# Performance work log

Measured on AMD Instinct MI355X. Metric: run time of the kernel, lower is better.

Reference implementation:

```python
import jax, jax.numpy as jnp
import numpy as np

N_SRC, N_TGT, E, L, C_OUT = 100000, 200000, 500000, 256, 2


def setup_inputs() -> dict:
    key = jax.random.key(0)
    ks = jax.random.split(key, 10)
    s = 1.0 / np.sqrt(L)
    return {
        "pos_source": jax.random.normal(ks[0], (N_SRC, 3), jnp.float32),
        "pos_target": jax.random.normal(ks[1], (N_TGT, 3), jnp.float32),
        "latents": jax.random.normal(ks[2], (N_SRC, L), jnp.float32),
        "row": jax.random.randint(ks[3], (E,), 0, N_TGT),
        "col": jax.random.randint(ks[4], (E,), 0, N_SRC),
        "W_in": jax.random.normal(ks[5], (L + 3, L), jnp.float32) * s,
        "b_in": jnp.zeros((L,), jnp.float32),
        "W1": jax.random.normal(ks[6], (L, L), jnp.float32) * s,
        "b1": jnp.zeros((L,), jnp.float32),
        "W2": jax.random.normal(ks[7], (L, L), jnp.float32) * s,
        "b2": jnp.zeros((L,), jnp.float32),
        "W_out": jax.random.normal(ks[8], (L, C_OUT), jnp.float32) * s,
        "b_out": jnp.zeros((C_OUT,), jnp.float32),
    }


def reference(pos_source, pos_target, latents, row, col,
              W_in, b_in, W1, b1, W2, b2, W_out, b_out):
    # gather relative positions and latents per neighbor pair: [E, 3], [E, L]
    pos_rel = pos_target[row] - pos_source[col]
    x = jnp.concatenate([latents[col], pos_rel], axis=1)  # [E, L+3]
    x = x @ W_in + b_in                                   # fc_in
    x = jax.nn.relu(x) @ W1 + b1                          # mlp layer 0 (act first)
    x = jax.nn.relu(x) @ W2 + b2                          # mlp layer 1
    x = x @ W_out + b_out                                 # fc_out (no activation)
    return x[:, 0]                                        # predictions
```

## Files before the change

### kernel.cpp

```cpp
#include <hip/hip_runtime.h>
#include <hip/hip_bf16.h>
#include <stdint.h>

typedef __attribute__((ext_vector_type(8))) short bf16x8;
typedef __attribute__((ext_vector_type(4))) float f32x4;

#define NSRC 100000
#define WIN_OFF 0
#define W1P_OFF (128*1024)
#define BU_OFF  (256*1024)
#define SS_OFF  (BU_OFF + 2048)
#define Y_OFF   (264*1024)

#define PAIRB 1040
#define XBYTES (32*PAIRB)
#define POFF(r) (((r)>>1)*PAIRB + ((r)&1)*512)

#define AS3U32(p) ((__attribute__((address_space(3))) uint32_t*)(uintptr_t)(p))
#define AS1U32(p) ((const __attribute__((address_space(1))) uint32_t*)(uintptr_t)(p))

__global__ __launch_bounds__(256) void pack_kernel(
    const float* __restrict__ Win, const float* __restrict__ W1,
    const float* __restrict__ W2, const float* __restrict__ Wout,
    const float* __restrict__ b1, const float* __restrict__ b2,
    const float* __restrict__ b_out, char* __restrict__ wp)
{
    const int t = threadIdx.x, blk = blockIdx.x;
    if (blk < 16) {
        const float* W = (blk < 8) ? Win : W1;
        char* dst = wp + ((blk < 8) ? WIN_OFF : W1P_OFF);
        const int c = blk & 7;
        #pragma unroll
        for (int q = 0; q < 4; ++q) {
            union { bf16x8 v; __hip_bfloat16 h[8]; } u;
            #pragma unroll
            for (int j = 0; j < 8; ++j)
                u.h[j] = __float2bfloat16(W[(size_t)(c*32 + q*8 + j)*256 + t]);
            *(bf16x8*)(dst + c*16384 + t*64 + q*16) = u.v;
        }
    } else if (blk < 24) {
        __shared__ float w0s[256];
        w0s[t] = Wout[t*2];
        __syncthreads();
        const int b = blk - 16, fl = t >> 3, sub = t & 7, f = b*32 + fl;
        const float* row = W2 + (size_t)f*256 + sub*32;
        float p = 0.f;
        #pragma unroll
        for (int j = 0; j < 32; ++j) p += row[j]*w0s[sub*32 + j];
        p += __shfl_xor(p,1); p += __shfl_xor(p,2); p += __shfl_xor(p,4);
        if (sub == 0) {
            float2 v; v.x = b1[f]; v.y = p;
            *(float2*)(wp + BU_OFF + f*8) = v;
        }
    } else {
        __shared__ float rb[4];
        float v = b2[t]*Wout[t*2];
        v += __shfl_xor(v,1); v += __shfl_xor(v,2); v += __shfl_xor(v,4);
        v += __shfl_xor(v,8); v += __shfl_xor(v,16); v += __shfl_xor(v,32);
        if ((t&63) == 0) rb[t>>6] = v;
        __syncthreads();
        if (t == 0) *(float*)(wp + SS_OFF) = rb[0]+rb[1]+rb[2]+rb[3] + b_out[0];
    }
}

__global__ __launch_bounds__(256, 2) void precompute_y(
    const float* __restrict__ latents, const float* __restrict__ b_in,
    const char* __restrict__ wp, char* __restrict__ Yc)
{
    __shared__ __align__(16) char Xs[XBYTES];
    __shared__ float binS[256];
    const int tid = threadIdx.x, wave = tid >> 6, lane = tid & 63;
    const int q = lane >> 4, lm = lane & 15;

    bf16x8 wA[4][8];
    {
        const char* wb = wp + WIN_OFF;
        #pragma unroll
        for (int mt = 0; mt < 4; ++mt) {
            const int m = wave*64 + mt*16 + lm;
            #pragma unroll
            for (int c = 0; c < 8; ++c)
                wA[mt][c] = *(const bf16x8*)(wb + c*16384 + m*64 + q*16);
        }
    }
    binS[tid] = b_in[tid];

    const int ntY = (NSRC + 63) / 64;
    for (int tile = blockIdx.x; tile < ntY; tile += 512) {
        const int base = tile*64;
        {
            const int r = tid & 63, h = tid >> 6;
            int srow = base + r; if (srow >= NSRC) srow = NSRC - 1;
            const float4* lp = (const float4*)(latents + (size_t)srow*256 + h*64);
            #pragma unroll
            for (int w = 0; w < 8; ++w) {
                float4 v0 = lp[w*2], v1 = lp[w*2+1];
                union { bf16x8 v; __hip_bfloat16 hh[8]; } u;
                u.hh[0]=__float2bfloat16(v0.x); u.hh[1]=__float2bfloat16(v0.y);
                u.hh[2]=__float2bfloat16(v0.z); u.hh[3]=__float2bfloat16(v0.w);
                u.hh[4]=__float2bfloat16(v1.x); u.hh[5]=__float2bfloat16(v1.y);
                u.hh[6]=__float2bfloat16(v1.z); u.hh[7]=__float2bfloat16(v1.w);
                *(bf16x8*)(Xs + POFF(r) + h*128 + w*16) = u.v;
            }
        }
        __syncthreads();
        f32x4 acc[4][4];
        #pragma unroll
        for (int mt = 0; mt < 4; ++mt)
            #pragma unroll
            for (int nt = 0; nt < 4; ++nt) acc[mt][nt] = (f32x4){0.f,0.f,0.f,0.f};
        #pragma unroll
        for (int c = 0; c < 8; ++c) {
            bf16x8 b[4];
            #pragma unroll
            for (int nt = 0; nt < 4; ++nt)
                b[nt] = *(const bf16x8*)(Xs + POFF(nt*16+lm) + c*64 + q*16);
            #pragma unroll
            for (int mt = 0; mt < 4; ++mt)
                #pragma unroll
                for (int nt = 0; nt < 4; ++nt)
                    acc[mt][nt] = __builtin_amdgcn_mfma_f32_16x16x32_bf16(wA[mt][c], b[nt], acc[mt][nt], 0,0,0);
        }
        #pragma unroll
        for (int mt = 0; mt < 4; ++mt) {
            const int f0 = wave*64 + mt*16 + q*4;
            float4 bb = *(const float4*)&binS[f0];
            float bbv[4] = {bb.x, bb.y, bb.z, bb.w};
            #pragma unroll
            for (int nt = 0; nt < 4; ++nt) {
                const int srow = base + nt*16 + lm;
                if (srow < NSRC) {
                    union { uint2 uu; __hip_bfloat16 hh[4]; } pk;
                    #pragma unroll
                    for (int rg = 0; rg < 4; ++rg)
                        pk.hh[rg] = __float2bfloat16(acc[mt][nt][rg] + bbv[rg]);
                    *(uint2*)(Yc + (size_t)srow*512 + f0*2) = pk.uu;
                }
            }
        }
        __syncthreads();
    }
}

__global__ __launch_bounds__(256, 2) void interp_main(
    const float* __restrict__ pos_src, const float* __restrict__ pos_tgt,
    const int* __restrict__ rowi, const int* __restrict__ coli,
    const float* __restrict__ Win, const char* __restrict__ wp,
    const char* __restrict__ Yc, float* __restrict__ out,
    int E, int ntiles)
{
    __shared__ __align__(16) char Xs[2][XBYTES];
    __shared__ float wposI[32][24];
    __shared__ float buS[512];
    __shared__ float posrel[2][64][4];
    __shared__ int   colsS[2][64];
    __shared__ float red[4][64];

    const int tid = threadIdx.x, wave = tid >> 6, lane = tid & 63;
    const int q = lane >> 4, lm = lane & 15;
    const int bid = blockIdx.x;

    bf16x8 wA[4][8];
    {
        const char* wb = wp + W1P_OFF;
        #pragma unroll
        for (int mt = 0; mt < 4; ++mt) {
            const int m = wave*64 + mt*16 + lm;
            #pragma unroll
            for (int c = 0; c < 8; ++c)
                wA[mt][c] = *(const bf16x8*)(wb + c*16384 + m*64 + q*16);
        }
    }
    {
        #pragma unroll
        for (int s = 0; s < 3; ++s)
            wposI[tid >> 3][s*8 + (tid & 7)] = Win[(size_t)(256+s)*256 + tid];
        *(float2*)&buS[tid*2] = *(const float2*)(wp + BU_OFF + tid*8);
    }
    const float Sv = *(const float*)(wp + SS_OFF);
    const int niter = (ntiles - bid + 511) / 512;

    #pragma unroll
    for (int ii = 0; ii < 2; ++ii) {
        if (tid < 64) {
            long tt = (long)bid + (long)ii*512; if (tt >= ntiles) tt = ntiles - 1;
            long e = tt*64 + tid; if (e >= E) e = E - 1;
            int ri = rowi[e], ci = coli[e];
            colsS[ii][tid] = ci;
            float4 pr;
            pr.x = pos_tgt[ri*3+0] - pos_src[ci*3+0];
            pr.y = pos_tgt[ri*3+1] - pos_src[ci*3+1];
            pr.z = pos_tgt[ri*3+2] - pos_src[ci*3+2];
            pr.w = 0.f;
            *(float4*)&posrel[ii][tid][0] = pr;
        }
    }
    __syncthreads();
    {
        #pragma unroll
        for (int k2 = 0; k2 < 8; ++k2) {
            const int r0 = wave*16 + k2*2;
            const int row = r0 + (lane >> 5);
            const int cv = colsS[0][row];
            const char* src = Yc + (size_t)cv*512 + (lane & 31)*16;
            __builtin_amdgcn_global_load_lds(AS1U32(src), AS3U32(Xs[0] + (r0>>1)*PAIRB), 16, 0, 0);
        }
    }

    for (int i = 0; i < niter; ++i) {
        const int p = i & 1;
        __syncthreads();

        if (i > 0 && tid < 64) {
            long e = ((long)bid + (long)(i-1)*512)*64 + tid;
            if (e < E) out[e] = red[0][tid]+red[1][tid]+red[2][tid]+red[3][tid] + Sv;
        }
        int m_ci = 0; float4 m_pr = {0.f,0.f,0.f,0.f};
        if (tid < 64) {
            long tt = (long)bid + (long)(i+2)*512; if (tt >= ntiles) tt = ntiles - 1;
            long e = tt*64 + tid; if (e >= E) e = E - 1;
            int ri = rowi[e]; m_ci = coli[e];
            m_pr.x = pos_tgt[ri*3+0] - pos_src[m_ci*3+0];
            m_pr.y = pos_tgt[ri*3+1] - pos_src[m_ci*3+1];
            m_pr.z = pos_tgt[ri*3+2] - pos_src[m_ci*3+2];
        }
        {
            const int fs = tid & 31, rb = tid >> 5;
            float w0v[8], w1v[8], w2v[8];
            {
                const float* wi = &wposI[fs][0];
                #pragma unroll
                for (int j = 0; j < 8; ++j) { w0v[j]=wi[j]; w1v[j]=wi[8+j]; w2v[j]=wi[16+j]; }
            }
            char* xb = Xs[p];
            #pragma unroll
            for (int ii2 = 0; ii2 < 8; ++ii2) {
                const int r = rb*8 + ii2;
                float4 pr = *(const float4*)&posrel[p][r][0];
                char* addr = xb + POFF(r) + fs*16;
                union { bf16x8 v; __hip_bfloat16 h[8]; } u;
                u.v = *(bf16x8*)addr;
                #pragma unroll
                for (int j = 0; j < 8; ++j) {
                    float vv = __bfloat162float(u.h[j]) + pr.x*w0v[j] + pr.y*w1v[j] + pr.z*w2v[j];
                    u.h[j] = __float2bfloat16(vv < 0.f ? 0.f : vv);
                }
                *(bf16x8*)addr = u.v;
            }
        }
        __syncthreads();

        {
            const int s = 1 - p;
            char* xb = Xs[s];
            #pragma unroll
            for (int k2 = 0; k2 < 8; ++k2) {
                const int r0 = wave*16 + k2*2;
                const int row = r0 + (lane >> 5);
                const int cv = colsS[s][row];
                const char* src = Yc + (size_t)cv*512 + (lane & 31)*16;
                __builtin_amdgcn_global_load_lds(AS1U32(src), AS3U32(xb + (r0>>1)*PAIRB), 16, 0, 0);
            }
        }
        f32x4 acc[4][4];
        #pragma unroll
        for (int mt = 0; mt < 4; ++mt)
            #pragma unroll
            for (int nt = 0; nt < 4; ++nt) acc[mt][nt] = (f32x4){0.f,0.f,0.f,0.f};
        {
            const char* xb = Xs[p];
            #pragma unroll
            for (int c = 0; c < 8; ++c) {
                bf16x8 b[4];
                #pragma unroll
                for (int nt = 0; nt < 4; ++nt)
                    b[nt] = *(const bf16x8*)(xb + POFF(nt*16+lm) + c*64 + q*16);
                #pragma unroll
                for (int mt = 0; mt < 4; ++mt)
                    #pragma unroll
                    for (int nt = 0; nt < 4; ++nt)
                        acc[mt][nt] = __builtin_amdgcn_mfma_f32_16x16x32_bf16(wA[mt][c], b[nt], acc[mt][nt], 0,0,0);
            }
        }
        float partial[4] = {0.f,0.f,0.f,0.f};
        #pragma unroll
        for (int mt = 0; mt < 4; ++mt) {
            const int f0 = wave*64 + mt*16 + q*4;
            float4 bu0 = *(const float4*)&buS[f0*2];
            float4 bu1 = *(const float4*)&buS[f0*2 + 4];
            float b1v[4] = {bu0.x, bu0.z, bu1.x, bu1.z};
            float uv[4]  = {bu0.y, bu0.w, bu1.y, bu1.w};
            #pragma unroll
            for (int nt = 0; nt < 4; ++nt)
                #pragma unroll
                for (int rg = 0; rg < 4; ++rg) {
                    float h = acc[mt][nt][rg] + b1v[rg];
                    if (h > 0.f) partial[nt] += h * uv[rg];
                }
        }
        #pragma unroll
        for (int nt = 0; nt < 4; ++nt) {
            float v = partial[nt];
            v += __shfl_xor(v, 16);
            v += __shfl_xor(v, 32);
            if (lane < 16) red[wave][nt*16 + lane] = v;
        }
        if (tid < 64) {
            colsS[p][tid] = m_ci;
            *(float4*)&posrel[p][tid][0] = m_pr;
        }
    }
    __syncthreads();
    if (tid < 64) {
        long e = ((long)bid + (long)(niter-1)*512)*64 + tid;
        if (e < E) out[e] = red[0][tid]+red[1][tid]+red[2][tid]+red[3][tid] + Sv;
    }
}

extern "C" void kernel_launch(void* const* d_in, const int* in_sizes, int n_in,
                              void* d_out, int out_size, void* d_ws, size_t ws_size,
                              hipStream_t stream)
{
    const float* pos_src = (const float*)d_in[0];
    const float* pos_tgt = (const float*)d_in[1];
    const float* latents = (const float*)d_in[2];
    const int*   rowi    = (const int*)d_in[3];
    const int*   coli    = (const int*)d_in[4];
    const float* Win     = (const float*)d_in[5];
    const float* b_in    = (const float*)d_in[6];
    const float* W1      = (const float*)d_in[7];
    const float* b1      = (const float*)d_in[8];
    const float* W2      = (const float*)d_in[9];
    const float* b2      = (const float*)d_in[10];
    const float* Wout    = (const float*)d_in[11];
    const float* b_out   = (const float*)d_in[12];
    float* out = (float*)d_out;
    const int E = in_sizes[3];
    const int ntiles = (E + 63) / 64;

    char* wp = (char*)d_ws;
    char* Yc = wp + Y_OFF;

    pack_kernel<<<25, 256, 0, stream>>>(Win, W1, W2, Wout, b1, b2, b_out, wp);
    precompute_y<<<512, 256, 0, stream>>>(latents, b_in, wp, Yc);
    interp_main<<<512, 256, 0, stream>>>(pos_src, pos_tgt, rowi, coli,
                                         Win, wp, Yc, out, E, ntiles);
}
```

Before: 311.2 us.

## Swizzle LDS tile layout and vectorize bf16 packing in interp kernels

```diff
diff --git a/kernel.cpp b/kernel.cpp
--- a/kernel.cpp
+++ b/kernel.cpp
@@ -12,12 +12,17 @@
 #define SS_OFF  (BU_OFF + 2048)
 #define Y_OFF   (264*1024)
 
-#define PAIRB 1040
-#define XBYTES (32*PAIRB)
-#define POFF(r) (((r)>>1)*PAIRB + ((r)&1)*512)
-
 #define AS3U32(p) ((__attribute__((address_space(3))) uint32_t*)(uintptr_t)(p))
 #define AS1U32(p) ((const __attribute__((address_space(1))) uint32_t*)(uintptr_t)(p))
+
+__device__ __forceinline__ int xpos(int r, int g) {
+    return (((g) & 24) | (((g) + (r)) & 7)) << 4;
+}
+
+__device__ __forceinline__ unsigned int pkbf16(float a, float b) {
+    __hip_bfloat162 h = __float22bfloat162_rn(make_float2(a, b));
+    union { __hip_bfloat162 h; unsigned int u; } c; c.h = h; return c.u;
+}
 
 __global__ __launch_bounds__(256) void pack_kernel(
     const float* __restrict__ Win, const float* __restrict__ W1,
@@ -49,8 +54,8 @@
         for (int j = 0; j < 32; ++j) p += row[j]*w0s[sub*32 + j];
         p += __shfl_xor(p,1); p += __shfl_xor(p,2); p += __shfl_xor(p,4);
         if (sub == 0) {
-            float2 v; v.x = b1[f]; v.y = p;
-            *(float2*)(wp + BU_OFF + f*8) = v;
+            *(float*)(wp + BU_OFF + f*4) = b1[f];
+            *(float*)(wp + BU_OFF + 1024 + f*4) = p;
         }
     } else {
         __shared__ float rb[4];
@@ -67,7 +72,7 @@
     const float* __restrict__ latents, const float* __restrict__ b_in,
     const char* __restrict__ wp, char* __restrict__ Yc)
 {
-    __shared__ __align__(16) char Xs[XBYTES];
+    __shared__ __align__(16) char Xs[64 * 512];
     __shared__ float binS[256];
     const int tid = threadIdx.x, wave = tid >> 6, lane = tid & 63;
     const int q = lane >> 4, lm = lane & 15;
@@ -88,20 +93,17 @@
     const int ntY = (NSRC + 63) / 64;
     for (int tile = blockIdx.x; tile < ntY; tile += 512) {
         const int base = tile*64;
-        {
-            const int r = tid & 63, h = tid >> 6;
+        #pragma unroll
+        for (int i = 0; i < 8; ++i) {
+            const int u = i*256 + tid;
+            const int r = u >> 5, g = u & 31;
             int srow = base + r; if (srow >= NSRC) srow = NSRC - 1;
-            const float4* lp = (const float4*)(latents + (size_t)srow*256 + h*64);
-            #pragma unroll
-            for (int w = 0; w < 8; ++w) {
-                float4 v0 = lp[w*2], v1 = lp[w*2+1];
-                union { bf16x8 v; __hip_bfloat16 hh[8]; } u;
-                u.hh[0]=__float2bfloat16(v0.x); u.hh[1]=__float2bfloat16(v0.y);
-                u.hh[2]=__float2bfloat16(v0.z); u.hh[3]=__float2bfloat16(v0.w);
-                u.hh[4]=__float2bfloat16(v1.x); u.hh[5]=__float2bfloat16(v1.y);
-                u.hh[6]=__float2bfloat16(v1.z); u.hh[7]=__float2bfloat16(v1.w);
-                *(bf16x8*)(Xs + POFF(r) + h*128 + w*16) = u.v;
-            }
+            const float4* lp = (const float4*)(latents + (size_t)srow*256 + g*8);
+            float4 v0 = lp[0], v1 = lp[1];
+            uint4 o;
+            o.x = pkbf16(v0.x, v0.y); o.y = pkbf16(v0.z, v0.w);
+            o.z = pkbf16(v1.x, v1.y); o.w = pkbf16(v1.z, v1.w);
+            *(uint4*)(Xs + r*512 + xpos(r, g)) = o;
         }
         __syncthreads();
         f32x4 acc[4][4];
@@ -113,8 +115,10 @@
         for (int c = 0; c < 8; ++c) {
             bf16x8 b[4];
             #pragma unroll
-            for (int nt = 0; nt < 4; ++nt)
-                b[nt] = *(const bf16x8*)(Xs + POFF(nt*16+lm) + c*64 + q*16);
+            for (int nt = 0; nt < 4; ++nt) {
+                const int r = nt*16 + lm;
+                b[nt] = *(const bf16x8*)(Xs + r*512 + xpos(r, c*4 + q));
+            }
             #pragma unroll
             for (int mt = 0; mt < 4; ++mt)
                 #pragma unroll
@@ -125,16 +129,14 @@
         for (int mt = 0; mt < 4; ++mt) {
             const int f0 = wave*64 + mt*16 + q*4;
             float4 bb = *(const float4*)&binS[f0];
-            float bbv[4] = {bb.x, bb.y, bb.z, bb.w};
             #pragma unroll
             for (int nt = 0; nt < 4; ++nt) {
                 const int srow = base + nt*16 + lm;
                 if (srow < NSRC) {
-                    union { uint2 uu; __hip_bfloat16 hh[4]; } pk;
-                    #pragma unroll
-                    for (int rg = 0; rg < 4; ++rg)
-                        pk.hh[rg] = __float2bfloat16(acc[mt][nt][rg] + bbv[rg]);
-                    *(uint2*)(Yc + (size_t)srow*512 + f0*2) = pk.uu;
+                    uint2 pk;
+                    pk.x = pkbf16(acc[mt][nt][0] + bb.x, acc[mt][nt][1] + bb.y);
+                    pk.y = pkbf16(acc[mt][nt][2] + bb.z, acc[mt][nt][3] + bb.w);
+                    *(uint2*)(Yc + (size_t)srow*512 + f0*2) = pk;
                 }
             }
         }
@@ -149,9 +151,9 @@
     const char* __restrict__ Yc, float* __restrict__ out,
     int E, int ntiles)
 {
-    __shared__ __align__(16) char Xs[2][XBYTES];
+    __shared__ __align__(16) char Xs[2][64 * 512];
     __shared__ float wposI[32][24];
-    __shared__ float buS[512];
+    __shared__ float b1S[256], uS[256];
     __shared__ float posrel[2][64][4];
     __shared__ int   colsS[2][64];
     __shared__ float red[4][64];
@@ -159,6 +161,7 @@
     const int tid = threadIdx.x, wave = tid >> 6, lane = tid & 63;
     const int q = lane >> 4, lm = lane & 15;
     const int bid = blockIdx.x;
+    const int p31 = lane & 31, h5 = lane >> 5;
 
     bf16x8 wA[4][8];
     {
@@ -175,7 +178,8 @@
         #pragma unroll
         for (int s = 0; s < 3; ++s)
             wposI[tid >> 3][s*8 + (tid & 7)] = Win[(size_t)(256+s)*256 + tid];
-        *(float2*)&buS[tid*2] = *(const float2*)(wp + BU_OFF + tid*8);
+        b1S[tid] = *(const float*)(wp + BU_OFF + tid*4);
+        uS[tid]  = *(const float*)(wp + BU_OFF + 1024 + tid*4);
     }
     const float Sv = *(const float*)(wp + SS_OFF);
     const int niter = (ntiles - bid + 511) / 512;
@@ -200,10 +204,23 @@
         #pragma unroll
         for (int k2 = 0; k2 < 8; ++k2) {
             const int r0 = wave*16 + k2*2;
-            const int row = r0 + (lane >> 5);
+            const int row = r0 + h5;
             const int cv = colsS[0][row];
-            const char* src = Yc + (size_t)cv*512 + (lane & 31)*16;
-            __builtin_amdgcn_global_load_lds(AS1U32(src), AS3U32(Xs[0] + (r0>>1)*PAIRB), 16, 0, 0);
+            const int g = (p31 & 24) | ((p31 - row) & 7);
+            const char* src = Yc + (size_t)cv*512 + g*16;
+            __builtin_amdgcn_global_load_lds(AS1U32(src), AS3U32(Xs[0] + r0*512), 16, 0, 0);
+        }
+    }
+
+    const int gR = tid & 31, rbR = tid >> 5;
+    float2 wx[4], wy[4], wz[4];
+    {
+        const float* wi = &wposI[gR][0];
+        #pragma unroll
+        for (int d = 0; d < 4; ++d) {
+            wx[d] = make_float2(wi[2*d],      wi[2*d+1]);
+            wy[d] = make_float2(wi[8+2*d],    wi[8+2*d+1]);
+            wz[d] = make_float2(wi[16+2*d],   wi[16+2*d+1]);
         }
     }
 
@@ -225,27 +242,27 @@
             m_pr.z = pos_tgt[ri*3+2] - pos_src[m_ci*3+2];
         }
         {
-            const int fs = tid & 31, rb = tid >> 5;
-            float w0v[8], w1v[8], w2v[8];
-            {
-                const float* wi = &wposI[fs][0];
+            char* xb = Xs[p];
+            #pragma unroll
+            for (int it = 0; it < 8; ++it) {
+                const int r = rbR*8 + it;
+                float4 pr = *(const float4*)&posrel[p][r][0];
+                char* addr = xb + r*512 + xpos(r, gR);
+                uint4 raw = *(uint4*)addr;
+                unsigned int rw[4] = {raw.x, raw.y, raw.z, raw.w};
+                uint4 o;
+                unsigned int ov[4];
                 #pragma unroll
-                for (int j = 0; j < 8; ++j) { w0v[j]=wi[j]; w1v[j]=wi[8+j]; w2v[j]=wi[16+j]; }
-            }
-            char* xb = Xs[p];
-            #pragma unroll
-            for (int ii2 = 0; ii2 < 8; ++ii2) {
-                const int r = rb*8 + ii2;
-                float4 pr = *(const float4*)&posrel[p][r][0];
-                char* addr = xb + POFF(r) + fs*16;
-                union { bf16x8 v; __hip_bfloat16 h[8]; } u;
-                u.v = *(bf16x8*)addr;
-                #pragma unroll
-                for (int j = 0; j < 8; ++j) {
-                    float vv = __bfloat162float(u.h[j]) + pr.x*w0v[j] + pr.y*w1v[j] + pr.z*w2v[j];
-                    u.h[j] = __float2bfloat16(vv < 0.f ? 0.f : vv);
+                for (int d = 0; d < 4; ++d) {
+                    float lo = __uint_as_float(rw[d] << 16);
+                    float hi = __uint_as_float(rw[d] & 0xffff0000u);
+                    float vx = fmaf(pr.z, wz[d].x, fmaf(pr.y, wy[d].x, fmaf(pr.x, wx[d].x, lo)));
+                    float vy = fmaf(pr.z, wz[d].y, fmaf(pr.y, wy[d].y, fmaf(pr.x, wx[d].y, hi)));
+                    vx = fmaxf(vx, 0.f); vy = fmaxf(vy, 0.f);
+                    ov[d] = pkbf16(vx, vy);
                 }
-                *(bf16x8*)addr = u.v;
+                o.x = ov[0]; o.y = ov[1]; o.z = ov[2]; o.w = ov[3];
+                *(uint4*)addr = o;
             }
         }
         __syncthreads();
@@ -256,10 +273,11 @@
             #pragma unroll
             for (int k2 = 0; k2 < 8; ++k2) {
                 const int r0 = wave*16 + k2*2;
-                const int row = r0 + (lane >> 5);
+                const int row = r0 + h5;
                 const int cv = colsS[s][row];
-                const char* src = Yc + (size_t)cv*512 + (lane & 31)*16;
-                __builtin_amdgcn_global_load_lds(AS1U32(src), AS3U32(xb + (r0>>1)*PAIRB), 16, 0, 0);
+                const int g = (p31 & 24) | ((p31 - row) & 7);
+                const char* src = Yc + (size_t)cv*512 + g*16;
+                __builtin_amdgcn_global_load_lds(AS1U32(src), AS3U32(xb + r0*512), 16, 0, 0);
             }
         }
         f32x4 acc[4][4];
@@ -273,8 +291,10 @@
             for (int c = 0; c < 8; ++c) {
                 bf16x8 b[4];
                 #pragma unroll
-                for (int nt = 0; nt < 4; ++nt)
-                    b[nt] = *(const bf16x8*)(xb + POFF(nt*16+lm) + c*64 + q*16);
+                for (int nt = 0; nt < 4; ++nt) {
+                    const int r = nt*16 + lm;
+                    b[nt] = *(const bf16x8*)(xb + r*512 + xpos(r, c*4 + q));
+                }
                 #pragma unroll
                 for (int mt = 0; mt < 4; ++mt)
                     #pragma unroll
@@ -282,25 +302,27 @@
                         acc[mt][nt] = __builtin_amdgcn_mfma_f32_16x16x32_bf16(wA[mt][c], b[nt], acc[mt][nt], 0,0,0);
             }
         }
-        float partial[4] = {0.f,0.f,0.f,0.f};
+        float2 p2[4] = {{0.f,0.f},{0.f,0.f},{0.f,0.f},{0.f,0.f}};
         #pragma unroll
         for (int mt = 0; mt < 4; ++mt) {
             const int f0 = wave*64 + mt*16 + q*4;
-            float4 bu0 = *(const float4*)&buS[f0*2];
-            float4 bu1 = *(const float4*)&buS[f0*2 + 4];
-            float b1v[4] = {bu0.x, bu0.z, bu1.x, bu1.z};
-            float uv[4]  = {bu0.y, bu0.w, bu1.y, bu1.w};
-            #pragma unroll
-            for (int nt = 0; nt < 4; ++nt)
-                #pragma unroll
-                for (int rg = 0; rg < 4; ++rg) {
-                    float h = acc[mt][nt][rg] + b1v[rg];
-                    if (h > 0.f) partial[nt] += h * uv[rg];
-                }
+            float2 bA = *(const float2*)&b1S[f0], bB = *(const float2*)&b1S[f0+2];
+            float2 uA = *(const float2*)&uS[f0],  uB = *(const float2*)&uS[f0+2];
+            #pragma unroll
+            for (int nt = 0; nt < 4; ++nt) {
+                float hx = fmaxf(acc[mt][nt][0] + bA.x, 0.f);
+                float hy = fmaxf(acc[mt][nt][1] + bA.y, 0.f);
+                float hz = fmaxf(acc[mt][nt][2] + bB.x, 0.f);
+                float hw = fmaxf(acc[mt][nt][3] + bB.y, 0.f);
+                p2[nt].x = fmaf(hx, uA.x, p2[nt].x);
+                p2[nt].y = fmaf(hy, uA.y, p2[nt].y);
+                p2[nt].x = fmaf(hz, uB.x, p2[nt].x);
+                p2[nt].y = fmaf(hw, uB.y, p2[nt].y);
+            }
         }
         #pragma unroll
         for (int nt = 0; nt < 4; ++nt) {
-            float v = partial[nt];
+            float v = p2[nt].x + p2[nt].y;
             v += __shfl_xor(v, 16);
             v += __shfl_xor(v, 32);
             if (lane < 16) red[wave][nt*16 + lane] = v;
```

Result: slower. 400.5 us (+28.7%).
